# Performance work log

Measured on AMD Instinct MI355X. Metric: run time of the kernel, lower is better.

The kernel has to match this reference:

```python
import jax, jax.numpy as jnp
import numpy as np

EPS = 1e-6
ROPE_THETA = 10000.0
NUM_HEADS = 32
NUM_KV_HEADS = 8
HEAD_DIM = 128
HIDDEN = 4096
B, S = 2, 2048


def setup_inputs() -> dict:
    key = jax.random.key(0)
    ks = jax.random.split(key, 6)
    scale = 0.02
    return {
        "hidden_states": jax.random.normal(ks[0], (B, S, HIDDEN), dtype=jnp.float32),
        "position_ids": jnp.arange(S, dtype=jnp.int64 if jax.config.jax_enable_x64 else jnp.int32)[None, :],
        "Wq": jax.random.normal(ks[1], (HIDDEN, NUM_HEADS * HEAD_DIM), dtype=jnp.float32) * scale,
        "Wk": jax.random.normal(ks[2], (HIDDEN, NUM_KV_HEADS * HEAD_DIM), dtype=jnp.float32) * scale,
        "Wv": jax.random.normal(ks[3], (HIDDEN, NUM_KV_HEADS * HEAD_DIM), dtype=jnp.float32) * scale,
        "Wo": jax.random.normal(ks[4], (NUM_HEADS * HEAD_DIM, HIDDEN), dtype=jnp.float32) * scale,
        "q_norm_w": jnp.ones((HEAD_DIM,), dtype=jnp.float32),
        "k_norm_w": jnp.ones((HEAD_DIM,), dtype=jnp.float32),
    }


def _rms_norm(x, w):
    # RMSNorm over last dim (head_dim)
    var = jnp.mean(jnp.square(x), axis=-1, keepdims=True)
    return x * jax.lax.rsqrt(var + EPS) * w


def _rope(x, position_ids):
    # x: [B, H, S, D]; Llama-style half-split rotation
    d = x.shape[-1]
    inv_freq = 1.0 / (ROPE_THETA ** (jnp.arange(0, d, 2, dtype=jnp.float32) / d))  # [D/2]
    ang = position_ids[:, :, None].astype(jnp.float32) * inv_freq[None, None, :]   # [B, S, D/2]
    emb = jnp.concatenate([ang, ang], axis=-1)                                     # [B, S, D]
    cos = jnp.cos(emb)[:, None, :, :]
    sin = jnp.sin(emb)[:, None, :, :]
    x1, x2 = x[..., : d // 2], x[..., d // 2:]
    rot = jnp.concatenate([-x2, x1], axis=-1)
    return x * cos + rot * sin


def reference(hidden_states, position_ids, Wq, Wk, Wv, Wo, q_norm_w, k_norm_w):
    b, s, _ = hidden_states.shape
    q = (hidden_states @ Wq).reshape(b, s, NUM_HEADS, HEAD_DIM).transpose(0, 2, 1, 3)
    k = (hidden_states @ Wk).reshape(b, s, NUM_KV_HEADS, HEAD_DIM).transpose(0, 2, 1, 3)
    v = (hidden_states @ Wv).reshape(b, s, NUM_KV_HEADS, HEAD_DIM).transpose(0, 2, 1, 3)

    q = _rms_norm(q, q_norm_w)
    k = _rms_norm(k, k_norm_w)

    q = _rope(q, position_ids)
    k = _rope(k, position_ids)

    groups = NUM_HEADS // NUM_KV_HEADS
    k = jnp.repeat(k, groups, axis=1)  # repeat_interleave along head dim
    v = jnp.repeat(v, groups, axis=1)

    scale = 1.0 / jnp.sqrt(jnp.float32(HEAD_DIM))
    scores = jnp.einsum("bhqd,bhkd->bhqk", q, k) * scale
    causal = jnp.tril(jnp.ones((s, s), dtype=bool))
    scores = jnp.where(causal[None, None], scores, jnp.finfo(scores.dtype).min)
    attn = jax.nn.softmax(scores, axis=-1)
    out = jnp.einsum("bhqk,bhkd->bhqd", attn, v)
    out = out.transpose(0, 2, 1, 3).reshape(b, s, NUM_HEADS * HEAD_DIM)
    return out @ Wo
```

## Files before the change

kernel.cpp:

```cpp
#include <hip/hip_runtime.h>
#include <stdint.h>
#include <stddef.h>

#define S_LEN 2048
#define BATCH 2
#define NHEADS 32
#define NKV 8
#define HD 128
#define HIDDEN 4096
#define T_TOK (BATCH * S_LEN)
#define QKV_W 6144

typedef unsigned short u16;
typedef __attribute__((ext_vector_type(4))) float f32x4;
typedef __attribute__((ext_vector_type(16))) float f32x16;
typedef __attribute__((ext_vector_type(8))) short s16x8;
typedef __attribute__((ext_vector_type(4))) unsigned short u16x4;
typedef __attribute__((ext_vector_type(4))) unsigned int u32x4;

__device__ __forceinline__ u16 f2bf(float f) {
  unsigned int u = __builtin_bit_cast(unsigned int, f);
  unsigned int r = (u + 0x7FFFu + ((u >> 16) & 1u)) >> 16;
  return (u16)r;
}
__device__ __forceinline__ float bf2f(u16 h) {
  return __builtin_bit_cast(float, ((unsigned int)h) << 16);
}

__device__ __forceinline__ void gload16(const void* g, void* l) {
  __builtin_amdgcn_global_load_lds((__attribute__((address_space(1))) void*)g,
                                   (__attribute__((address_space(3))) void*)l,
                                   16, 0, 0);
}

__device__ __forceinline__ unsigned cvtpk(float a, float b) {
  unsigned r;
  asm("v_cvt_pk_bf16_f32 %0, %1, %2" : "=v"(r) : "v"(a), "v"(b));
  return r;
}
__device__ __forceinline__ void lohi_dup(unsigned W, unsigned& lo, unsigned& hi) {
  unsigned a = W, b = W;
  asm volatile("v_permlane32_swap_b32 %0, %1" : "+v"(a), "+v"(b));
  lo = a; hi = b;
}

__global__ __launch_bounds__(256) void k_convert(const float* __restrict__ in,
                                                 u16* __restrict__ out, int n8) {
  int i = blockIdx.x * 256 + threadIdx.x;
  if (i >= n8) return;
  float4 a = ((const float4*)in)[i * 2];
  float4 b = ((const float4*)in)[i * 2 + 1];
  u16x4 lo = {f2bf(a.x), f2bf(a.y), f2bf(a.z), f2bf(a.w)};
  u16x4 hi = {f2bf(b.x), f2bf(b.y), f2bf(b.z), f2bf(b.w)};
  ((u16x4*)out)[i * 2] = lo;
  ((u16x4*)out)[i * 2 + 1] = hi;
}

__global__ __launch_bounds__(256) void k_transpose_w(const float* __restrict__ W,
                                                     u16* __restrict__ Wt, int K,
                                                     int N, int outRowOff,
                                                     int outStride) {
  __shared__ float tl[32][33];
  int k0 = blockIdx.x * 32, n0 = blockIdx.y * 32;
  int t = threadIdx.x;
  int r = t >> 3, c4 = (t & 7) * 4;
  float4 v = *(const float4*)&W[(size_t)(k0 + r) * N + n0 + c4];
  tl[r][c4] = v.x; tl[r][c4 + 1] = v.y; tl[r][c4 + 2] = v.z; tl[r][c4 + 3] = v.w;
  __syncthreads();
  u16x4 o = {f2bf(tl[c4][r]), f2bf(tl[c4 + 1][r]), f2bf(tl[c4 + 2][r]),
             f2bf(tl[c4 + 3][r])};
  *(u16x4*)&Wt[(size_t)(outRowOff + n0 + r) * outStride + k0 + c4] = o;
}

__global__ __launch_bounds__(256) void k_rope_tab(const int* __restrict__ pos,
                                                  float* __restrict__ tab) {
  int i = blockIdx.x * 256 + threadIdx.x;
  int s = i >> 6, l = i & 63;
  float p = (float)pos[s];
  float ang = p * expf(-(float)l * 0.14391156516342163f);
  tab[s * 128 + l] = cosf(ang);
  tab[s * 128 + 64 + l] = sinf(ang);
}

template <typename OutT>
__global__ __launch_bounds__(512, 2) void k_gemm8p(const u16* __restrict__ A,
                                                   const u16* __restrict__ Bt,
                                                   OutT* __restrict__ C,
                                                   int N, int K) {
  __shared__ u16 As[2][16384];
  __shared__ u16 Bs[2][16384];
  int nbn = N >> 8;
  int nwg = gridDim.x;
  int orig = blockIdx.x;
  int q8 = nwg >> 3, r8 = nwg & 7;
  int xcd = orig & 7, sub = orig >> 3;
  int wgid = (xcd < r8 ? xcd * (q8 + 1) : r8 * (q8 + 1) + (xcd - r8) * q8) + sub;
  int bm = wgid / nbn, bn = wgid % nbn;
  int tid = threadIdx.x, wid = tid >> 6, lane = tid & 63;
  int wm = wid >> 2, wn = wid & 3;
  int g = lane >> 4, c = lane & 15;
  int l3 = lane >> 3, l7 = lane & 7;
  int swz = c & 7;
  int xunit = (l7 ^ l3) * 8;

  f32x4 acc[8][4];
#pragma unroll
  for (int m = 0; m < 8; m++)
#pragma unroll
    for (int n = 0; n < 4; n++) acc[m][n] = (f32x4){0.f, 0.f, 0.f, 0.f};

  const u16* aBase = A + (size_t)(bm * 256 + wid * 16 + l3) * K + xunit;
  const u16* bBase = Bt + (size_t)(bn * 256 + wid * 16 + l3) * K + xunit;

  auto stgA = [&](int buf, int h, size_t koff) {
    gload16(aBase + (size_t)(h * 128) * K + koff,
            &As[buf][(h * 128 + wid * 16) * 64]);
    gload16(aBase + (size_t)(h * 128 + 8) * K + koff,
            &As[buf][(h * 128 + wid * 16 + 8) * 64]);
  };
  auto stgB = [&](int buf, int h, size_t koff) {
    gload16(bBase + (size_t)(h * 128) * K + koff,
            &Bs[buf][(h * 128 + wid * 16) * 64]);
    gload16(bBase + (size_t)(h * 128 + 8) * K + koff,
            &Bs[buf][(h * 128 + wid * 16 + 8) * 64]);
  };

  s16x8 af[4][2], bf0[2][2], bf1[2][2];
  auto rdA = [&](int buf, int mh) {
#pragma unroll
    for (int mi = 0; mi < 4; mi++)
#pragma unroll
      for (int ks = 0; ks < 2; ks++)
        af[mi][ks] = *(const s16x8*)&As[buf][(wm * 128 + mh * 64 + mi * 16 + c) * 64 +
                                            (((ks * 4 + g) ^ swz) * 8)];
  };
  auto rdB = [&](int buf, int nh, s16x8 (&bf)[2][2]) {
#pragma unroll
    for (int nj = 0; nj < 2; nj++)
#pragma unroll
      for (int ks = 0; ks < 2; ks++)
        bf[nj][ks] = *(const s16x8*)&Bs[buf][(wn * 64 + nh * 32 + nj * 16 + c) * 64 +
                                            (((ks * 4 + g) ^ swz) * 8)];
  };
  auto quad = [&](int mh, int nh, s16x8 (&bf)[2][2]) {
    __builtin_amdgcn_s_setprio(1);
#pragma unroll
    for (int mi = 0; mi < 4; mi++)
#pragma unroll
      for (int nj = 0; nj < 2; nj++)
#pragma unroll
        for (int ks = 0; ks < 2; ks++)
          acc[mh * 4 + mi][nh * 2 + nj] = __builtin_amdgcn_mfma_f32_16x16x32_bf16(
              af[mi][ks], bf[nj][ks], acc[mh * 4 + mi][nh * 2 + nj], 0, 0, 0);
    __builtin_amdgcn_s_setprio(0);
  };
#define BAR() __builtin_amdgcn_s_barrier()
#define LGKM0() asm volatile("s_waitcnt lgkmcnt(0)" ::: "memory")
#define VM(n) asm volatile("s_waitcnt vmcnt(" #n ")" ::: "memory")

  int nt2 = K >> 7;
  stgB(0, 0, 0); stgB(0, 1, 0);
  stgA(0, 0, 0); stgA(0, 1, 0);
  stgB(1, 0, 64); stgB(1, 1, 64);
  VM(4);
  BAR();

  for (int j = 0; j < nt2; j++) {
    size_t k1 = (size_t)(2 * j + 1) << 6;
    size_t k2 = (size_t)(2 * j + 2) << 6;
    size_t k3 = (size_t)(2 * j + 3) << 6;
    bool st = (j + 1 < nt2);
    rdA(0, 0); rdB(0, 0, bf0);
    stgA(1, 0, k1);
    BAR(); LGKM0();
    quad(0, 0, bf0);
    BAR();
    rdB(0, 1, bf1);
    stgA(1, 1, k1);
    BAR(); LGKM0();
    quad(0, 1, bf1);
    BAR();
    rdA(0, 1);
    if (st) stgB(0, 0, k2);
    BAR(); LGKM0();
    quad(1, 0, bf0);
    BAR();
    if (st) stgB(0, 1, k2);
    BAR(); LGKM0();
    quad(1, 1, bf1);
    if (st) { VM(4); } else { VM(0); }
    BAR();
    rdA(1, 0); rdB(1, 0, bf0);
    if (st) stgA(0, 0, k2);
    BAR(); LGKM0();
    quad(0, 0, bf0);
    BAR();
    rdB(1, 1, bf1);
    if (st) stgA(0, 1, k2);
    BAR(); LGKM0();
    quad(0, 1, bf1);
    BAR();
    rdA(1, 1);
    if (st) stgB(1, 0, k3);
    BAR(); LGKM0();
    quad(1, 0, bf0);
    BAR();
    if (st) stgB(1, 1, k3);
    BAR(); LGKM0();
    quad(1, 1, bf1);
    if (st) { VM(4); }
    BAR();
  }
#undef BAR
#undef LGKM0
#undef VM

#pragma unroll
  for (int m = 0; m < 8; m++)
#pragma unroll
    for (int n = 0; n < 4; n++) {
      size_t row = (size_t)bm * 256 + wm * 128 + m * 16 + g * 4;
      size_t col = (size_t)bn * 256 + wn * 64 + n * 16 + c;
#pragma unroll
      for (int r = 0; r < 4; r++) {
        float v = acc[m][n][r];
        if constexpr (sizeof(OutT) == 2)
          C[(row + r) * N + col] = (OutT)f2bf(v);
        else
          C[(row + r) * N + col] = (OutT)v;
      }
    }
}

__global__ __launch_bounds__(256) void k_rmsrope(u16* __restrict__ QK,
                                                 const float* __restrict__ w,
                                                 const float* __restrict__ tab,
                                                 int H, int rowStride) {
  int row = blockIdx.x * 4 + (threadIdx.x >> 6);
  int lane = threadIdx.x & 63;
  int t = row / H, h = row - t * H;
  int s = t & (S_LEN - 1);
  u16* p = QK + (size_t)t * rowStride + h * HD;
  float x1 = bf2f(p[lane]), x2 = bf2f(p[lane + 64]);
  float ss = x1 * x1 + x2 * x2;
#pragma unroll
  for (int o = 32; o >= 1; o >>= 1) ss += __shfl_xor(ss, o);
  float inv = rsqrtf(ss * (1.0f / 128.0f) + 1e-6f);
  float y1 = x1 * inv * w[lane], y2 = x2 * inv * w[lane + 64];
  float cs = tab[s * 128 + lane], sn = tab[s * 128 + 64 + lane];
  p[lane] = f2bf(y1 * cs - y2 * sn);
  p[lane + 64] = f2bf(y2 * cs + y1 * sn);
}

__global__ __launch_bounds__(256) void k_transpose_v(const u16* __restrict__ QKV,
                                                     u16* __restrict__ Vt) {
  __shared__ u16 tl[32][40];
  int bkh = blockIdx.x;
  int s0 = blockIdx.y * 32, d0 = blockIdx.z * 32;
  int b = bkh >> 3, kh = bkh & 7;
  int t = threadIdx.x, r = t >> 3, c4 = (t & 7) * 4;
  const u16* src =
      QKV + (size_t)(b * S_LEN + s0 + r) * QKV_W + 5120 + kh * HD + d0 + c4;
  u16x4 v = *(const u16x4*)src;
  tl[r][c4] = v[0]; tl[r][c4 + 1] = v[1]; tl[r][c4 + 2] = v[2]; tl[r][c4 + 3] = v[3];
  __syncthreads();
  u16x4 o = {tl[c4][r], tl[c4 + 1][r], tl[c4 + 2][r], tl[c4 + 3][r]};
  *(u16x4*)&Vt[(size_t)(bkh * HD + d0 + r) * S_LEN + s0 + c4] = o;
}

__global__ __launch_bounds__(256) void k_attn(const u16* __restrict__ QKV,
                                              const u16* __restrict__ Vt,
                                              u16* __restrict__ Oact) {
  __shared__ u16 Ks[2][64 * 128];
  __shared__ u16 Vs[2][128 * 64];
  int bid = blockIdx.x;
  int xcd = bid & 7, slot = bid >> 3;
  int grp = xcd * 2 + (slot >> 5);
  int b = grp >> 3, kh = grp & 7;
  int s32 = slot & 31;
  int pr = s32 >> 2;
  int h = kh * 4 + (s32 & 3);
  int w = threadIdx.x >> 6, lane = threadIdx.x & 63;
  int q31 = lane & 31, hh = lane >> 5;
  const float qscale = 0.12751740810f;

  const char* Kg = (const char*)(QKV + (size_t)b * S_LEN * QKV_W + 4096 + kh * HD);
  const char* Vg = (const char*)(Vt + (size_t)(b * 8 + kh) * HD * S_LEN);

#pragma unroll 1
  for (int half = 0; half < 2; half++) {
    __syncthreads();
    int qt = half ? 15 - pr : pr;
    int qw0 = qt * 128 + w * 32;

    s16x8 qf[8];
    const u16* Qp = QKV + (size_t)(b * S_LEN + qw0 + q31) * QKV_W + h * HD + hh * 8;
#pragma unroll
    for (int dc = 0; dc < 8; dc++) {
      s16x8 raw = *(const s16x8*)(Qp + dc * 16);
#pragma unroll
      for (int e = 0; e < 8; e++)
        qf[dc][e] = (short)f2bf(bf2f((u16)raw[e]) * qscale);
    }

    f32x16 o[4];
#pragma unroll
    for (int d = 0; d < 4; d++)
#pragma unroll
      for (int r = 0; r < 16; r++) o[d][r] = 0.f;
    float m = -3.0e38f, l = 0.f;

    int nch = 2 * qt + 2;

    {
      char* KsB = (char*)Ks[0];
      char* VsB = (char*)Vs[0];
#pragma unroll
      for (int j = 0; j < 4; j++) {
        int ins = w * 4 + j;
        int row = ins * 4 + (lane >> 4);
        int bc = ((lane & 15) * 16) ^ ((row & 7) << 4);
        gload16(Kg + (size_t)row * 12288 + bc, KsB + ins * 1024);
      }
#pragma unroll
      for (int j = 0; j < 4; j++) {
        int ins = w * 4 + j;
        int row = ins * 8 + (lane >> 3);
        int bc = ((lane & 7) * 16) ^ ((row & 7) << 4);
        gload16(Vg + (size_t)row * 4096 + bc, VsB + ins * 1024);
      }
    }

    int cur = 0;
    for (int ch = 0; ch < nch; ch++) {
      int kb = ch * 64;
      __syncthreads();
      if (ch + 1 < nch) {
        char* KsB = (char*)Ks[cur ^ 1];
        char* VsB = (char*)Vs[cur ^ 1];
        int kb2 = kb + 64;
#pragma unroll
        for (int j = 0; j < 4; j++) {
          int ins = w * 4 + j;
          int row = ins * 4 + (lane >> 4);
          int bc = ((lane & 15) * 16) ^ ((row & 7) << 4);
          gload16(Kg + (size_t)(kb2 + row) * 12288 + bc, KsB + ins * 1024);
        }
#pragma unroll
        for (int j = 0; j < 4; j++) {
          int ins = w * 4 + j;
          int row = ins * 8 + (lane >> 3);
          int bc = ((lane & 7) * 16) ^ ((row & 7) << 4);
          gload16(Vg + (size_t)row * 4096 + (size_t)kb2 * 2 + bc, VsB + ins * 1024);
        }
      }
      if (kb <= qw0 + 31) {
        char* KsB = (char*)Ks[cur];
        char* VsB = (char*)Vs[cur];
        f32x16 sA, sB;
#pragma unroll
        for (int r = 0; r < 16; r++) { sA[r] = 0.f; sB[r] = 0.f; }
        int sw = (q31 & 7) << 4;
        __builtin_amdgcn_s_setprio(1);
#pragma unroll
        for (int dc = 0; dc < 8; dc++) {
          s16x8 kfA = *(const s16x8*)(KsB + q31 * 256 + ((dc * 32 + hh * 16) ^ sw));
          s16x8 kfB = *(const s16x8*)(KsB + (32 + q31) * 256 + ((dc * 32 + hh * 16) ^ sw));
          sA = __builtin_amdgcn_mfma_f32_32x32x16_bf16(kfA, qf[dc], sA, 0, 0, 0);
          sB = __builtin_amdgcn_mfma_f32_32x32x16_bf16(kfB, qf[dc], sB, 0, 0, 0);
        }
        __builtin_amdgcn_s_setprio(0);
        if (kb + 63 > qw0) {
          int qa = qw0 + q31;
#pragma unroll
          for (int r = 0; r < 16; r++) {
            int krow = (r & 3) + 8 * (r >> 2) + 4 * hh;
            if (kb + krow > qa) sA[r] = -1e30f;
            if (kb + 32 + krow > qa) sB[r] = -1e30f;
          }
        }
        float mx = -3.0e38f;
#pragma unroll
        for (int r = 0; r < 16; r++) mx = fmaxf(mx, fmaxf(sA[r], sB[r]));
        mx = fmaxf(mx, __shfl_xor(mx, 32));
        if (!__all(mx - m <= 11.5f)) {
          float mnew = fmaxf(m, mx);
          float corr = __builtin_amdgcn_exp2f(m - mnew);
          l *= corr;
#pragma unroll
          for (int d = 0; d < 4; d++)
#pragma unroll
            for (int r = 0; r < 16; r++) o[d][r] *= corr;
          m = mnew;
        }
        float rs = 0.f;
#pragma unroll
        for (int r = 0; r < 16; r++) {
          sA[r] = __builtin_amdgcn_exp2f(sA[r] - m); rs += sA[r];
          sB[r] = __builtin_amdgcn_exp2f(sB[r] - m); rs += sB[r];
        }
        rs += __shfl_xor(rs, 32);
        l += rs;
#pragma unroll
        for (int st = 0; st < 2; st++) {
          unsigned Aw[8], Bw[8];
#pragma unroll
          for (int j = 0; j < 8; j++) {
            float p0 = st ? sB[2 * j] : sA[2 * j];
            float p1 = st ? sB[2 * j + 1] : sA[2 * j + 1];
            lohi_dup(cvtpk(p0, p1), Aw[j], Bw[j]);
          }
#pragma unroll
          for (int kc2 = 0; kc2 < 2; kc2++) {
            u32x4 wv;
            wv.x = hh ? Aw[kc2 * 4 + 2] : Aw[kc2 * 4 + 0];
            wv.y = hh ? Aw[kc2 * 4 + 3] : Aw[kc2 * 4 + 1];
            wv.z = hh ? Bw[kc2 * 4 + 2] : Bw[kc2 * 4 + 0];
            wv.w = hh ? Bw[kc2 * 4 + 3] : Bw[kc2 * 4 + 1];
            s16x8 pf = __builtin_bit_cast(s16x8, wv);
            int kc = st * 2 + kc2;
            __builtin_amdgcn_s_setprio(1);
#pragma unroll
            for (int d = 0; d < 4; d++) {
              int row = d * 32 + q31;
              int vsw = (row & 7) << 4;
              s16x8 vf = *(const s16x8*)(VsB + row * 128 + ((kc * 32 + hh * 16) ^ vsw));
              o[d] = __builtin_amdgcn_mfma_f32_32x32x16_bf16(vf, pf, o[d], 0, 0, 0);
            }
            __builtin_amdgcn_s_setprio(0);
          }
        }
      }
      cur ^= 1;
    }
    float linv = 1.0f / l;
    u16* Op = Oact + (size_t)(b * S_LEN + qw0 + q31) * 4096 + h * HD;
#pragma unroll
    for (int d = 0; d < 4; d++)
#pragma unroll
      for (int g4 = 0; g4 < 4; g4++) {
        int d0 = d * 32 + 8 * g4 + 4 * hh;
        u16x4 w4 = {f2bf(o[d][4 * g4 + 0] * linv), f2bf(o[d][4 * g4 + 1] * linv),
                    f2bf(o[d][4 * g4 + 2] * linv), f2bf(o[d][4 * g4 + 3] * linv)};
        *(u16x4*)(Op + d0) = w4;
      }
  }
}

extern "C" void kernel_launch(void* const* d_in, const int* in_sizes, int n_in,
                              void* d_out, int out_size, void* d_ws,
                              size_t ws_size, hipStream_t stream) {
  (void)in_sizes; (void)n_in; (void)out_size; (void)ws_size;
  const float* X = (const float*)d_in[0];
  const int* pos = (const int*)d_in[1];
  const float* Wq = (const float*)d_in[2];
  const float* Wk = (const float*)d_in[3];
  const float* Wv = (const float*)d_in[4];
  const float* Wo = (const float*)d_in[5];
  const float* qw = (const float*)d_in[6];
  const float* kw = (const float*)d_in[7];
  float* out = (float*)d_out;
  char* ws = (char*)d_ws;

  const size_t MB = 1024ull * 1024ull;
  u16* Xb    = (u16*)(ws + 0 * MB);
  u16* WqkvT = (u16*)(ws + 32 * MB);
  u16* WkvT  = (u16*)(ws + 64 * MB);
  u16* WoT   = (u16*)(ws + 80 * MB);
  u16* QKV   = (u16*)(ws + 112 * MB);
  u16* Vt    = (u16*)(ws + 160 * MB);
  u16* Oact  = (u16*)(ws + 168 * MB);
  float* tab = (float*)(ws + 200 * MB);

  k_convert<<<8192, 256, 0, stream>>>(X, Xb, (T_TOK * HIDDEN) / 8);
  k_transpose_w<<<dim3(128, 128), 256, 0, stream>>>(Wq, WqkvT, 4096, 4096, 0, 4096);
  k_transpose_w<<<dim3(128, 32), 256, 0, stream>>>(Wk, WkvT, 4096, 1024, 0, 4096);
  k_transpose_w<<<dim3(128, 32), 256, 0, stream>>>(Wv, WkvT, 4096, 1024, 1024, 4096);
  k_transpose_w<<<dim3(128, 128), 256, 0, stream>>>(Wo, WoT, 4096, 4096, 0, 4096);
  k_rope_tab<<<512, 256, 0, stream>>>(pos, tab);

  k_gemm8p<u16><<<16 * 24, 512, 0, stream>>>(Xb, WqkvT, QKV, QKV_W, 4096);

  k_rmsrope<<<(T_TOK * NHEADS) / 4, 256, 0, stream>>>(QKV, qw, tab, NHEADS, QKV_W);
  k_rmsrope<<<(T_TOK * NKV) / 4, 256, 0, stream>>>(QKV + 4096, kw, tab, NKV, QKV_W);

  k_transpose_v<<<dim3(16, 64, 4), 256, 0, stream>>>(QKV, Vt);

  k_attn<<<512, 256, 0, stream>>>(QKV, Vt, Oact);

  k_gemm8p<float><<<16 * 16, 512, 0, stream>>>(Oact, WoT, out, 4096, 4096);
}
```

Before: 643.2 us.

## Restructure GEMM main loop to halve barriers and double-buffer A fragments

The bf16 GEMM inner loop now loads all B fragments and a second A fragment set into registers up front, removes the explicit lgkmcnt(0) waits, and drops half of the workgroup barriers per K step. Scheduling barriers are added after each s_barrier so the compiler cannot move LDS reads across them. Launch bounds no longer request two blocks per CU, which frees registers for the extra fragment arrays. The aim is to cut synchronization stalls and let LDS reads overlap MFMA work, at the cost of more register pressure and possibly lower occupancy.

```diff
diff --git a/kernel.cpp b/kernel.cpp
--- a/kernel.cpp
+++ b/kernel.cpp
@@ -83,10 +83,10 @@
 }
 
 template <typename OutT>
-__global__ __launch_bounds__(512, 2) void k_gemm8p(const u16* __restrict__ A,
-                                                   const u16* __restrict__ Bt,
-                                                   OutT* __restrict__ C,
-                                                   int N, int K) {
+__global__ __launch_bounds__(512) void k_gemm8p(const u16* __restrict__ A,
+                                                const u16* __restrict__ Bt,
+                                                OutT* __restrict__ C,
+                                                int N, int K) {
   __shared__ u16 As[2][16384];
   __shared__ u16 Bs[2][16384];
   int nbn = N >> 8;
@@ -125,24 +125,24 @@
             &Bs[buf][(h * 128 + wid * 16 + 8) * 64]);
   };
 
-  s16x8 af[4][2], bf0[2][2], bf1[2][2];
-  auto rdA = [&](int buf, int mh) {
+  s16x8 af[4][2], af2[4][2], bf0[2][2], bf1[2][2];
+  auto rdA = [&](s16x8 (&d)[4][2], int buf, int mh) {
 #pragma unroll
     for (int mi = 0; mi < 4; mi++)
 #pragma unroll
       for (int ks = 0; ks < 2; ks++)
-        af[mi][ks] = *(const s16x8*)&As[buf][(wm * 128 + mh * 64 + mi * 16 + c) * 64 +
-                                            (((ks * 4 + g) ^ swz) * 8)];
+        d[mi][ks] = *(const s16x8*)&As[buf][(wm * 128 + mh * 64 + mi * 16 + c) * 64 +
+                                           (((ks * 4 + g) ^ swz) * 8)];
   };
-  auto rdB = [&](int buf, int nh, s16x8 (&bf)[2][2]) {
+  auto rdB = [&](s16x8 (&d)[2][2], int buf, int nh) {
 #pragma unroll
     for (int nj = 0; nj < 2; nj++)
 #pragma unroll
       for (int ks = 0; ks < 2; ks++)
-        bf[nj][ks] = *(const s16x8*)&Bs[buf][(wn * 64 + nh * 32 + nj * 16 + c) * 64 +
-                                            (((ks * 4 + g) ^ swz) * 8)];
+        d[nj][ks] = *(const s16x8*)&Bs[buf][(wn * 64 + nh * 32 + nj * 16 + c) * 64 +
+                                           (((ks * 4 + g) ^ swz) * 8)];
   };
-  auto quad = [&](int mh, int nh, s16x8 (&bf)[2][2]) {
+  auto quad = [&](s16x8 (&a)[4][2], s16x8 (&bf)[2][2], int mh, int nh) {
     __builtin_amdgcn_s_setprio(1);
 #pragma unroll
     for (int mi = 0; mi < 4; mi++)
@@ -151,11 +151,14 @@
 #pragma unroll
         for (int ks = 0; ks < 2; ks++)
           acc[mh * 4 + mi][nh * 2 + nj] = __builtin_amdgcn_mfma_f32_16x16x32_bf16(
-              af[mi][ks], bf[nj][ks], acc[mh * 4 + mi][nh * 2 + nj], 0, 0, 0);
+              a[mi][ks], bf[nj][ks], acc[mh * 4 + mi][nh * 2 + nj], 0, 0, 0);
     __builtin_amdgcn_s_setprio(0);
   };
-#define BAR() __builtin_amdgcn_s_barrier()
-#define LGKM0() asm volatile("s_waitcnt lgkmcnt(0)" ::: "memory")
+#define BAR()                          \
+  do {                                 \
+    __builtin_amdgcn_s_barrier();      \
+    __builtin_amdgcn_sched_barrier(0); \
+  } while (0)
 #define VM(n) asm volatile("s_waitcnt vmcnt(" #n ")" ::: "memory")
 
   int nt2 = K >> 7;
@@ -170,49 +173,38 @@
     size_t k2 = (size_t)(2 * j + 2) << 6;
     size_t k3 = (size_t)(2 * j + 3) << 6;
     bool st = (j + 1 < nt2);
-    rdA(0, 0); rdB(0, 0, bf0);
+    rdA(af, 0, 0); rdB(bf0, 0, 0); rdB(bf1, 0, 1);
     stgA(1, 0, k1);
-    BAR(); LGKM0();
-    quad(0, 0, bf0);
-    BAR();
-    rdB(0, 1, bf1);
+    quad(af, bf0, 0, 0);
+    BAR();
+    rdA(af2, 0, 1);
     stgA(1, 1, k1);
-    BAR(); LGKM0();
-    quad(0, 1, bf1);
-    BAR();
-    rdA(0, 1);
+    quad(af, bf1, 0, 1);
+    BAR();
     if (st) stgB(0, 0, k2);
-    BAR(); LGKM0();
-    quad(1, 0, bf0);
+    quad(af2, bf0, 1, 0);
     BAR();
     if (st) stgB(0, 1, k2);
-    BAR(); LGKM0();
-    quad(1, 1, bf1);
+    quad(af2, bf1, 1, 1);
     if (st) { VM(4); } else { VM(0); }
     BAR();
-    rdA(1, 0); rdB(1, 0, bf0);
+    rdA(af, 1, 0); rdB(bf0, 1, 0); rdB(bf1, 1, 1);
     if (st) stgA(0, 0, k2);
-    BAR(); LGKM0();
-    quad(0, 0, bf0);
-    BAR();
-    rdB(1, 1, bf1);
+    quad(af, bf0, 0, 0);
+    BAR();
+    rdA(af2, 1, 1);
     if (st) stgA(0, 1, k2);
-    BAR(); LGKM0();
-    quad(0, 1, bf1);
-    BAR();
-    rdA(1, 1);
+    quad(af, bf1, 0, 1);
+    BAR();
     if (st) stgB(1, 0, k3);
-    BAR(); LGKM0();
-    quad(1, 0, bf0);
+    quad(af2, bf0, 1, 0);
     BAR();
     if (st) stgB(1, 1, k3);
-    BAR(); LGKM0();
-    quad(1, 1, bf1);
+    quad(af2, bf1, 1, 1);
     if (st) { VM(4); }
     BAR();
   }
 #undef BAR
-#undef LGKM0
 #undef VM
 
 #pragma unroll
```

Result: slower. 679.1 us (+5.6%).
